# Kernel optimization log

Measured on AMD Instinct MI355X. Metric: run time of the kernel, lower is better.

Reference implementation:

```python
import jax, jax.numpy as jnp
import numpy as np

B, S, D_IN, D_OUT = 4, 2048, 1024, 1024


def setup_inputs() -> dict:
    key = jax.random.key(0)
    k1, k2, k3, k4 = jax.random.split(key, 4)
    scale = 1.0 / np.sqrt(D_IN)
    return {
        "x": jax.random.normal(k1, (B, S, D_IN), dtype=jnp.float32),
        "W_q": jax.random.normal(k2, (D_OUT, D_IN), dtype=jnp.float32) * scale,
        "W_k": jax.random.normal(k3, (D_OUT, D_IN), dtype=jnp.float32) * scale,
        "W_v": jax.random.normal(k4, (D_OUT, D_IN), dtype=jnp.float32) * scale,
    }


def reference(x, W_q, W_k, W_v):
    # torch nn.Linear: y = x @ W.T (bias=False)
    q = jnp.einsum("bsd,od->bso", x, W_q)
    k = jnp.einsum("bsd,od->bso", x, W_k)
    v = jnp.einsum("bsd,od->bso", x, W_v)
    s = q.shape[1]
    scores = jnp.einsum("bqo,bko->bqk", q, k)  # [B, S, S]
    causal = jnp.triu(jnp.ones((s, s), dtype=bool), k=1)
    scores = jnp.where(causal, -jnp.inf, scores)
    inv_sqrt_d = 1.0 / jnp.sqrt(jnp.asarray(q.shape[-1], scores.dtype))
    attn = jax.nn.softmax(scores * inv_sqrt_d, axis=-1)
    # dropout p=0.0 -> identity (deterministic reference)
    return jnp.einsum("bqk,bko->bqo", attn, v)
```

## Files before the change

### kernel.cpp

```cpp
#include <hip/hip_runtime.h>

typedef unsigned short u16;
typedef __bf16 bf16x8 __attribute__((ext_vector_type(8)));
typedef float f32x4 __attribute__((ext_vector_type(4)));

#define AS1 __attribute__((address_space(1)))
#define AS3 __attribute__((address_space(3)))

__device__ inline u16 f2bf(float f) {
  union { float f; unsigned u; } a; a.f = f;
  unsigned u = a.u;
  return (u16)((u + 0x7fffu + ((u >> 16) & 1u)) >> 16);
}

__global__ __launch_bounds__(256) void cvt_kernel(const float* __restrict__ in,
                                                  u16* __restrict__ out) {
  size_t i = ((size_t)blockIdx.x * 256 + threadIdx.x) * 4;
  float4 v = *(const float4*)(in + i);
  ushort4 o;
  o.x = f2bf(v.x); o.y = f2bf(v.y); o.z = f2bf(v.z); o.w = f2bf(v.w);
  *(ushort4*)(out + i) = o;
}

__global__ __launch_bounds__(256) void cvt3_kernel(
    const float* __restrict__ a, const float* __restrict__ b, const float* __restrict__ c,
    u16* __restrict__ oa, u16* __restrict__ ob, u16* __restrict__ oc) {
  int bid = blockIdx.x;
  const float* in; u16* out;
  if (bid < 1024) { in = a; out = oa; }
  else if (bid < 2048) { in = b; out = ob; bid -= 1024; }
  else { in = c; out = oc; bid -= 2048; }
  size_t i = ((size_t)bid * 256 + threadIdx.x) * 4;
  float4 v = *(const float4*)(in + i);
  ushort4 o;
  o.x = f2bf(v.x); o.y = f2bf(v.y); o.z = f2bf(v.z); o.w = f2bf(v.w);
  *(ushort4*)(out + i) = o;
}

template <typename CT>
__device__ __forceinline__ void gemm_core(
    const u16* __restrict__ A, const u16* __restrict__ B, CT* __restrict__ C,
    int nt, int lda, int ldb, int ldc, int m0, int n0, bool atom) {
  __shared__ __align__(16) u16 lds[65536];

  const int tid = threadIdx.x;
  const int ln = tid & 63, wv = tid >> 6;
  const int wr = wv >> 2, wc = wv & 3;

  auto stage = [&](const u16* src, int ld, int t, int h, int ldsbase) {
#pragma unroll
    for (int i = 0; i < 2; ++i) {
      const int c = h * 1024 + i * 512 + tid;
      const int row = c >> 3, slot = c & 7;
      const int col = (slot ^ (row & 7)) * 8;
      __builtin_amdgcn_global_load_lds(
          (const AS1 void*)(src + (size_t)row * ld + (size_t)t * 64 + col),
          (AS3 void*)(&lds[ldsbase + c * 8]), 16, 0, 0);
    }
  };

  f32x4 acc[8][4] = {};

  stage(B, ldb, 0, 0, 32768); stage(B, ldb, 0, 1, 32768);
  stage(A, lda, 0, 0, 0);     stage(A, lda, 0, 1, 0);
  if (nt > 1) {
    stage(B, ldb, 1, 0, 32768 + 16384); stage(B, ldb, 1, 1, 32768 + 16384);
    stage(A, lda, 1, 0, 16384);         stage(A, lda, 1, 1, 16384);
    asm volatile("s_waitcnt vmcnt(8)" ::: "memory");
  } else {
    asm volatile("s_waitcnt vmcnt(0)" ::: "memory");
  }
  __builtin_amdgcn_s_barrier();

  for (int t = 0; t < nt; ++t) {
    const int p = t & 1;
    const u16* La = &lds[p * 16384];
    const u16* Lb = &lds[32768 + p * 16384];
    bf16x8 bfr[4][2];
#pragma unroll
    for (int q = 0; q < 4; ++q) {
      if (q == 0) {
        __builtin_amdgcn_sched_barrier(0);
#pragma unroll
        for (int ni = 0; ni < 4; ++ni)
#pragma unroll
          for (int ks = 0; ks < 2; ++ks) {
            const int row = wc * 64 + ni * 16 + (ln & 15);
            const int kc = ks * 4 + (ln >> 4);
            bfr[ni][ks] = *(const bf16x8*)&Lb[row * 64 + ((kc ^ (row & 7)) << 3)];
          }
      }
      bf16x8 afr[2][2];
#pragma unroll
      for (int mi = 0; mi < 2; ++mi)
#pragma unroll
        for (int ks = 0; ks < 2; ++ks) {
          const int row = wr * 128 + (q * 2 + mi) * 16 + (ln & 15);
          const int kc = ks * 4 + (ln >> 4);
          afr[mi][ks] = *(const bf16x8*)&La[row * 64 + ((kc ^ (row & 7)) << 3)];
        }
      if (q == 0)      { if (t >= 1 && t + 1 < nt) stage(A, lda, t + 1, 0, (p ^ 1) * 16384); }
      else if (q == 1) { if (t >= 1 && t + 1 < nt) stage(A, lda, t + 1, 1, (p ^ 1) * 16384); }
      else if (q == 2) { if (t + 2 < nt) stage(B, ldb, t + 2, 0, 32768 + p * 16384); }
      else             { if (t + 2 < nt) stage(B, ldb, t + 2, 1, 32768 + p * 16384); }

      __builtin_amdgcn_s_barrier();
      __builtin_amdgcn_s_setprio(1);
#pragma unroll
      for (int mi = 0; mi < 2; ++mi)
#pragma unroll
        for (int ni = 0; ni < 4; ++ni)
#pragma unroll
          for (int ks = 0; ks < 2; ++ks)
            acc[q * 2 + mi][ni] = __builtin_amdgcn_mfma_f32_16x16x32_bf16(
                afr[mi][ks], bfr[ni][ks], acc[q * 2 + mi][ni], 0, 0, 0);
      __builtin_amdgcn_s_setprio(0);
      if (q == 3) {
        if (t + 2 < nt)      asm volatile("s_waitcnt vmcnt(4)" ::: "memory");
        else if (t + 1 < nt) asm volatile("s_waitcnt vmcnt(0)" ::: "memory");
      }
      __builtin_amdgcn_s_barrier();
    }
  }

#pragma unroll
  for (int mi = 0; mi < 8; ++mi) {
    const int rbase = m0 + wr * 128 + mi * 16 + (ln >> 4) * 4;
#pragma unroll
    for (int ni = 0; ni < 4; ++ni) {
      const int col = n0 + wc * 64 + ni * 16 + (ln & 15);
#pragma unroll
      for (int r = 0; r < 4; ++r) {
        const float v = acc[mi][ni][r];
        CT* ptr = &C[(size_t)(rbase + r) * ldc + col];
        if constexpr (sizeof(CT) == 4) {
          if (atom) atomicAdd((float*)ptr, v);
          else *(float*)ptr = v;
        } else {
          *ptr = f2bf(v);
        }
      }
    }
  }
}

__global__ __launch_bounds__(512, 2) void proj_kernel(
    const u16* __restrict__ xb, const u16* __restrict__ wqb,
    const u16* __restrict__ wkb, const u16* __restrict__ wvb,
    u16* __restrict__ Qb, u16* __restrict__ Kb, u16* __restrict__ VTb) {
  const int bid = blockIdx.x;
  const u16 *A, *B;
  u16* C;
  int ldc, m0, n0;
  if (bid < 256) {
    const int w = bid >> 7, r = bid & 127;
    m0 = (r >> 2) * 256; n0 = (r & 3) * 256;
    A = xb; B = w ? wkb : wqb; C = w ? Kb : Qb; ldc = 1024;
  } else {
    int r = bid - 256;
    const int z = r >> 5; r &= 31;
    m0 = (r >> 3) * 256; n0 = (r & 7) * 256;
    A = wvb; B = xb + (size_t)z * 2048 * 1024; C = VTb + (size_t)z * 1024 * 2048;
    ldc = 2048;
  }
  gemm_core<u16>(A + (size_t)m0 * 1024, B + (size_t)n0 * 1024, C, 16, 1024, 1024, ldc, m0, n0, false);
}

__global__ __launch_bounds__(512, 2) void qkt_kernel(
    const u16* __restrict__ Qb, const u16* __restrict__ Kb, float* __restrict__ Sb) {
  const int x = blockIdx.x;
  int mi = 0;
  while ((mi + 1) * (mi + 2) / 2 <= x) ++mi;
  const int ni = x - mi * (mi + 1) / 2;
  const int m0 = mi * 256, n0 = ni * 256;
  const u16* A = Qb + (size_t)blockIdx.y * 2048 * 1024 + (size_t)m0 * 1024;
  const u16* B = Kb + (size_t)blockIdx.y * 2048 * 1024 + (size_t)n0 * 1024;
  float* C = Sb + (size_t)blockIdx.y * 2048 * 2048;
  gemm_core<float>(A, B, C, 16, 1024, 1024, 2048, m0, n0, false);
}

__global__ __launch_bounds__(512, 2) void pv_kernel(
    const u16* __restrict__ P, const u16* __restrict__ VTb, float* __restrict__ out) {
  const int c = blockIdx.x;
  int m, k0, ntc; bool atom;
  if (c < 4) { m = c; k0 = 0; ntc = 4 * (c + 1); atom = false; }
  else {
    const int j = c - 4;
    m = 4 + (j >> 1);
    const int nth = 2 * (m + 1);
    k0 = (j & 1) * nth; ntc = nth; atom = true;
  }
  const int m0 = m * 256, n0 = blockIdx.y * 256;
  const u16* A = P + (size_t)blockIdx.z * 2048 * 4096 + (size_t)m0 * 4096 + (size_t)k0 * 64;
  const u16* B = VTb + (size_t)blockIdx.z * 1024 * 2048 + (size_t)n0 * 2048 + (size_t)k0 * 64;
  float* C = out + (size_t)blockIdx.z * 2048 * 1024;
  gemm_core<float>(A, B, C, ntc, 4096, 2048, 1024, m0, n0, atom);
}

__global__ __launch_bounds__(256) void softmax_kernel(float* __restrict__ S, float scale) {
  const int q = blockIdx.x;
  float* row = S + ((size_t)blockIdx.y * 2048 + q) * 2048;
  const int t = threadIdx.x;
  float4 v0 = *(const float4*)(row + t * 4);
  float4 v1 = *(const float4*)(row + 1024 + t * 4);
  float x[8] = {v0.x, v0.y, v0.z, v0.w, v1.x, v1.y, v1.z, v1.w};
  float m = -3.4e38f;
#pragma unroll
  for (int i = 0; i < 8; ++i) {
    const int j = (i < 4) ? (t * 4 + i) : (1024 + t * 4 + (i - 4));
    x[i] = (j <= q) ? x[i] * scale : -3.4e38f;
    m = fmaxf(m, x[i]);
  }
#pragma unroll
  for (int off = 32; off > 0; off >>= 1) m = fmaxf(m, __shfl_xor(m, off, 64));
  __shared__ float redm[4], reds[4];
  const int ln = t & 63, wv = t >> 6;
  if (ln == 0) redm[wv] = m;
  __syncthreads();
  m = fmaxf(fmaxf(redm[0], redm[1]), fmaxf(redm[2], redm[3]));

  float p[8];
  float s = 0.f;
#pragma unroll
  for (int i = 0; i < 8; ++i) {
    p[i] = __expf(x[i] - m);
    s += p[i];
  }
#pragma unroll
  for (int off = 32; off > 0; off >>= 1) s += __shfl_xor(s, off, 64);
  if (ln == 0) reds[wv] = s;
  __syncthreads();
  s = reds[0] + reds[1] + reds[2] + reds[3];
  const float r = 1.0f / s;

  u16* prow = (u16*)row;
  ushort4 o0, o1;
  o0.x = f2bf(p[0] * r); o0.y = f2bf(p[1] * r); o0.z = f2bf(p[2] * r); o0.w = f2bf(p[3] * r);
  o1.x = f2bf(p[4] * r); o1.y = f2bf(p[5] * r); o1.z = f2bf(p[6] * r); o1.w = f2bf(p[7] * r);
  *(ushort4*)(prow + t * 4) = o0;
  *(ushort4*)(prow + 1024 + t * 4) = o1;
}

extern "C" void kernel_launch(void* const* d_in, const int* in_sizes, int n_in,
                              void* d_out, int out_size, void* d_ws, size_t ws_size,
                              hipStream_t stream) {
  const float* x  = (const float*)d_in[0];
  const float* Wq = (const float*)d_in[1];
  const float* Wk = (const float*)d_in[2];
  const float* Wv = (const float*)d_in[3];
  float* out = (float*)d_out;

  char* ws = (char*)d_ws;
  u16* xb   = (u16*)(ws);
  u16* wqb  = (u16*)(ws + (16ul << 20));
  u16* wkb  = (u16*)(ws + (18ul << 20));
  u16* wvb  = (u16*)(ws + (20ul << 20));
  u16* Qb   = (u16*)(ws + (22ul << 20));
  u16* Kb   = (u16*)(ws + (38ul << 20));
  u16* VTb  = (u16*)(ws + (54ul << 20));
  float* Sb = (float*)(ws + (70ul << 20));

  hipMemsetAsync(out, 0, (size_t)out_size * 4, stream);

  cvt_kernel<<<8192, 256, 0, stream>>>(x, xb);
  cvt3_kernel<<<3072, 256, 0, stream>>>(Wq, Wk, Wv, wqb, wkb, wvb);

  proj_kernel<<<384, 512, 0, stream>>>(xb, wqb, wkb, wvb, Qb, Kb, VTb);

  qkt_kernel<<<dim3(36, 4), 512, 0, stream>>>(Qb, Kb, Sb);

  softmax_kernel<<<dim3(2048, 4), 256, 0, stream>>>(Sb, 0.03125f);

  pv_kernel<<<dim3(12, 4, 4), 512, 0, stream>>>((const u16*)Sb, VTb, out);
}
```

Baseline: 175.6 us.

## Split V projection into a 128-row-tile kernel and trim causal softmax and memset work

The GEMM core is templated on the M tile size (256 or 128) so LDS buffers, staging sweeps, wait counts and accumulators scale with it. The V^T projection moves into its own kernel with 128-row tiles, giving 256 blocks instead of 128. The aim is better CU load balance than the previous 384-block combined launch. Softmax rows with q<1024 no longer load or write the upper half, which the causal PV kernel never reads. The output memset now clears only the rows that are accumulated atomically. In exchange there is one extra kernel launch, and the V tiles are smaller, with less reuse per tile.

```diff
diff --git a/kernel.cpp b/kernel.cpp
--- a/kernel.cpp
+++ b/kernel.cpp
@@ -37,36 +37,41 @@
   *(ushort4*)(out + i) = o;
 }
 
-template <typename CT>
+template <typename CT, int BM>
 __device__ __forceinline__ void gemm_core(
     const u16* __restrict__ A, const u16* __restrict__ B, CT* __restrict__ C,
     int nt, int lda, int ldb, int ldc, int m0, int n0, bool atom) {
-  __shared__ __align__(16) u16 lds[65536];
+  constexpr int ABUF = BM * 64;
+  constexpr int ASW = BM / 64;
+  constexpr int PH_MI = BM / 128;
+  __shared__ __align__(16) u16 lds[2 * ABUF + 32768];
 
   const int tid = threadIdx.x;
   const int ln = tid & 63, wv = tid >> 6;
   const int wr = wv >> 2, wc = wv & 3;
 
-  auto stage = [&](const u16* src, int ld, int t, int h, int ldsbase) {
-#pragma unroll
-    for (int i = 0; i < 2; ++i) {
-      const int c = h * 1024 + i * 512 + tid;
-      const int row = c >> 3, slot = c & 7;
-      const int col = (slot ^ (row & 7)) * 8;
-      __builtin_amdgcn_global_load_lds(
-          (const AS1 void*)(src + (size_t)row * ld + (size_t)t * 64 + col),
-          (AS3 void*)(&lds[ldsbase + c * 8]), 16, 0, 0);
-    }
+  auto sweep = [&](const u16* src, int ld, int t, int s, int base) {
+    const int c = s * 512 + tid;
+    const int row = c >> 3, slot = c & 7;
+    const int col = (slot ^ (row & 7)) * 8;
+    __builtin_amdgcn_global_load_lds(
+        (const AS1 void*)(src + (size_t)row * ld + (size_t)t * 64 + col),
+        (AS3 void*)(&lds[base + c * 8]), 16, 0, 0);
   };
 
-  f32x4 acc[8][4] = {};
-
-  stage(B, ldb, 0, 0, 32768); stage(B, ldb, 0, 1, 32768);
-  stage(A, lda, 0, 0, 0);     stage(A, lda, 0, 1, 0);
+  f32x4 acc[2 * BM / 64][4] = {};
+
+#pragma unroll
+  for (int s = 0; s < 4; ++s) sweep(B, ldb, 0, s, 2 * ABUF);
+#pragma unroll
+  for (int s = 0; s < ASW; ++s) sweep(A, lda, 0, s, 0);
   if (nt > 1) {
-    stage(B, ldb, 1, 0, 32768 + 16384); stage(B, ldb, 1, 1, 32768 + 16384);
-    stage(A, lda, 1, 0, 16384);         stage(A, lda, 1, 1, 16384);
-    asm volatile("s_waitcnt vmcnt(8)" ::: "memory");
+#pragma unroll
+    for (int s = 0; s < 4; ++s) sweep(B, ldb, 1, s, 2 * ABUF + 16384);
+#pragma unroll
+    for (int s = 0; s < ASW; ++s) sweep(A, lda, 1, s, ABUF);
+    if constexpr (ASW == 4) asm volatile("s_waitcnt vmcnt(8)" ::: "memory");
+    else                    asm volatile("s_waitcnt vmcnt(6)" ::: "memory");
   } else {
     asm volatile("s_waitcnt vmcnt(0)" ::: "memory");
   }
@@ -74,8 +79,8 @@
 
   for (int t = 0; t < nt; ++t) {
     const int p = t & 1;
-    const u16* La = &lds[p * 16384];
-    const u16* Lb = &lds[32768 + p * 16384];
+    const u16* La = &lds[p * ABUF];
+    const u16* Lb = &lds[2 * ABUF + p * 16384];
     bf16x8 bfr[4][2];
 #pragma unroll
     for (int q = 0; q < 4; ++q) {
@@ -90,30 +95,36 @@
             bfr[ni][ks] = *(const bf16x8*)&Lb[row * 64 + ((kc ^ (row & 7)) << 3)];
           }
       }
-      bf16x8 afr[2][2];
-#pragma unroll
-      for (int mi = 0; mi < 2; ++mi)
+      bf16x8 afr[PH_MI][2];
+#pragma unroll
+      for (int mi = 0; mi < PH_MI; ++mi)
 #pragma unroll
         for (int ks = 0; ks < 2; ++ks) {
-          const int row = wr * 128 + (q * 2 + mi) * 16 + (ln & 15);
+          const int row = wr * (BM / 2) + (q * PH_MI + mi) * 16 + (ln & 15);
           const int kc = ks * 4 + (ln >> 4);
           afr[mi][ks] = *(const bf16x8*)&La[row * 64 + ((kc ^ (row & 7)) << 3)];
         }
-      if (q == 0)      { if (t >= 1 && t + 1 < nt) stage(A, lda, t + 1, 0, (p ^ 1) * 16384); }
-      else if (q == 1) { if (t >= 1 && t + 1 < nt) stage(A, lda, t + 1, 1, (p ^ 1) * 16384); }
-      else if (q == 2) { if (t + 2 < nt) stage(B, ldb, t + 2, 0, 32768 + p * 16384); }
-      else             { if (t + 2 < nt) stage(B, ldb, t + 2, 1, 32768 + p * 16384); }
+      if constexpr (PH_MI == 2) {
+        if (q == 0)      { if (t >= 1 && t + 1 < nt) { sweep(A, lda, t + 1, 0, (p ^ 1) * ABUF); sweep(A, lda, t + 1, 1, (p ^ 1) * ABUF); } }
+        else if (q == 1) { if (t >= 1 && t + 1 < nt) { sweep(A, lda, t + 1, 2, (p ^ 1) * ABUF); sweep(A, lda, t + 1, 3, (p ^ 1) * ABUF); } }
+        else if (q == 2) { if (t + 2 < nt) { sweep(B, ldb, t + 2, 0, 2 * ABUF + p * 16384); sweep(B, ldb, t + 2, 1, 2 * ABUF + p * 16384); } }
+        else             { if (t + 2 < nt) { sweep(B, ldb, t + 2, 2, 2 * ABUF + p * 16384); sweep(B, ldb, t + 2, 3, 2 * ABUF + p * 16384); } }
+      } else {
+        if (q == 0)      { if (t >= 1 && t + 1 < nt) { sweep(A, lda, t + 1, 0, (p ^ 1) * ABUF); sweep(A, lda, t + 1, 1, (p ^ 1) * ABUF); } }
+        else if (q == 2) { if (t + 2 < nt) { sweep(B, ldb, t + 2, 0, 2 * ABUF + p * 16384); sweep(B, ldb, t + 2, 1, 2 * ABUF + p * 16384); } }
+        else if (q == 3) { if (t + 2 < nt) { sweep(B, ldb, t + 2, 2, 2 * ABUF + p * 16384); sweep(B, ldb, t + 2, 3, 2 * ABUF + p * 16384); } }
+      }
 
       __builtin_amdgcn_s_barrier();
       __builtin_amdgcn_s_setprio(1);
 #pragma unroll
-      for (int mi = 0; mi < 2; ++mi)
+      for (int mi = 0; mi < PH_MI; ++mi)
 #pragma unroll
         for (int ni = 0; ni < 4; ++ni)
 #pragma unroll
           for (int ks = 0; ks < 2; ++ks)
-            acc[q * 2 + mi][ni] = __builtin_amdgcn_mfma_f32_16x16x32_bf16(
-                afr[mi][ks], bfr[ni][ks], acc[q * 2 + mi][ni], 0, 0, 0);
+            acc[q * PH_MI + mi][ni] = __builtin_amdgcn_mfma_f32_16x16x32_bf16(
+                afr[mi][ks], bfr[ni][ks], acc[q * PH_MI + mi][ni], 0, 0, 0);
       __builtin_amdgcn_s_setprio(0);
       if (q == 3) {
         if (t + 2 < nt)      asm volatile("s_waitcnt vmcnt(4)" ::: "memory");
@@ -124,8 +135,8 @@
   }
 
 #pragma unroll
-  for (int mi = 0; mi < 8; ++mi) {
-    const int rbase = m0 + wr * 128 + mi * 16 + (ln >> 4) * 4;
+  for (int mi = 0; mi < 2 * BM / 64; ++mi) {
+    const int rbase = m0 + wr * (BM / 2) + mi * 16 + (ln >> 4) * 4;
 #pragma unroll
     for (int ni = 0; ni < 4; ++ni) {
       const int col = n0 + wc * 64 + ni * 16 + (ln & 15);
@@ -144,26 +155,26 @@
   }
 }
 
-__global__ __launch_bounds__(512, 2) void proj_kernel(
+__global__ __launch_bounds__(512, 2) void proj_qk_kernel(
     const u16* __restrict__ xb, const u16* __restrict__ wqb,
-    const u16* __restrict__ wkb, const u16* __restrict__ wvb,
-    u16* __restrict__ Qb, u16* __restrict__ Kb, u16* __restrict__ VTb) {
+    const u16* __restrict__ wkb, u16* __restrict__ Qb, u16* __restrict__ Kb) {
   const int bid = blockIdx.x;
-  const u16 *A, *B;
-  u16* C;
-  int ldc, m0, n0;
-  if (bid < 256) {
-    const int w = bid >> 7, r = bid & 127;
-    m0 = (r >> 2) * 256; n0 = (r & 3) * 256;
-    A = xb; B = w ? wkb : wqb; C = w ? Kb : Qb; ldc = 1024;
-  } else {
-    int r = bid - 256;
-    const int z = r >> 5; r &= 31;
-    m0 = (r >> 3) * 256; n0 = (r & 7) * 256;
-    A = wvb; B = xb + (size_t)z * 2048 * 1024; C = VTb + (size_t)z * 1024 * 2048;
-    ldc = 2048;
-  }
-  gemm_core<u16>(A + (size_t)m0 * 1024, B + (size_t)n0 * 1024, C, 16, 1024, 1024, ldc, m0, n0, false);
+  const int w = bid >> 7, r = bid & 127;
+  const int m0 = (r >> 2) * 256, n0 = (r & 3) * 256;
+  const u16* B = w ? wkb : wqb;
+  u16* C = w ? Kb : Qb;
+  gemm_core<u16, 256>(xb + (size_t)m0 * 1024, B + (size_t)n0 * 1024, C,
+                      16, 1024, 1024, 1024, m0, n0, false);
+}
+
+__global__ __launch_bounds__(512, 2) void vt_kernel(
+    const u16* __restrict__ wvb, const u16* __restrict__ xb, u16* __restrict__ VTb) {
+  const int z = blockIdx.x >> 6, r = blockIdx.x & 63;
+  const int m0 = (r >> 3) * 128, n0 = (r & 7) * 256;
+  gemm_core<u16, 128>(wvb + (size_t)m0 * 1024,
+                      xb + (size_t)z * 2048 * 1024 + (size_t)n0 * 1024,
+                      VTb + (size_t)z * 1024 * 2048,
+                      16, 1024, 1024, 2048, m0, n0, false);
 }
 
 __global__ __launch_bounds__(512, 2) void qkt_kernel(
@@ -176,7 +187,7 @@
   const u16* A = Qb + (size_t)blockIdx.y * 2048 * 1024 + (size_t)m0 * 1024;
   const u16* B = Kb + (size_t)blockIdx.y * 2048 * 1024 + (size_t)n0 * 1024;
   float* C = Sb + (size_t)blockIdx.y * 2048 * 2048;
-  gemm_core<float>(A, B, C, 16, 1024, 1024, 2048, m0, n0, false);
+  gemm_core<float, 256>(A, B, C, 16, 1024, 1024, 2048, m0, n0, false);
 }
 
 __global__ __launch_bounds__(512, 2) void pv_kernel(
@@ -194,15 +205,16 @@
   const u16* A = P + (size_t)blockIdx.z * 2048 * 4096 + (size_t)m0 * 4096 + (size_t)k0 * 64;
   const u16* B = VTb + (size_t)blockIdx.z * 1024 * 2048 + (size_t)n0 * 2048 + (size_t)k0 * 64;
   float* C = out + (size_t)blockIdx.z * 2048 * 1024;
-  gemm_core<float>(A, B, C, ntc, 4096, 2048, 1024, m0, n0, atom);
+  gemm_core<float, 256>(A, B, C, ntc, 4096, 2048, 1024, m0, n0, atom);
 }
 
 __global__ __launch_bounds__(256) void softmax_kernel(float* __restrict__ S, float scale) {
   const int q = blockIdx.x;
+  const bool full = (q >= 1024);
   float* row = S + ((size_t)blockIdx.y * 2048 + q) * 2048;
   const int t = threadIdx.x;
   float4 v0 = *(const float4*)(row + t * 4);
-  float4 v1 = *(const float4*)(row + 1024 + t * 4);
+  float4 v1 = full ? *(const float4*)(row + 1024 + t * 4) : float4{0, 0, 0, 0};
   float x[8] = {v0.x, v0.y, v0.z, v0.w, v1.x, v1.y, v1.z, v1.w};
   float m = -3.4e38f;
 #pragma unroll
@@ -236,9 +248,11 @@
   u16* prow = (u16*)row;
   ushort4 o0, o1;
   o0.x = f2bf(p[0] * r); o0.y = f2bf(p[1] * r); o0.z = f2bf(p[2] * r); o0.w = f2bf(p[3] * r);
-  o1.x = f2bf(p[4] * r); o1.y = f2bf(p[5] * r); o1.z = f2bf(p[6] * r); o1.w = f2bf(p[7] * r);
   *(ushort4*)(prow + t * 4) = o0;
-  *(ushort4*)(prow + 1024 + t * 4) = o1;
+  if (full) {
+    o1.x = f2bf(p[4] * r); o1.y = f2bf(p[5] * r); o1.z = f2bf(p[6] * r); o1.w = f2bf(p[7] * r);
+    *(ushort4*)(prow + 1024 + t * 4) = o1;
+  }
 }
 
 extern "C" void kernel_launch(void* const* d_in, const int* in_sizes, int n_in,
@@ -260,12 +274,14 @@
   u16* VTb  = (u16*)(ws + (54ul << 20));
   float* Sb = (float*)(ws + (70ul << 20));
 
-  hipMemsetAsync(out, 0, (size_t)out_size * 4, stream);
+  for (int b = 0; b < 4; ++b)
+    hipMemsetAsync(out + ((size_t)b * 2048 + 1024) * 1024, 0, 1024 * 1024 * 4, stream);
 
   cvt_kernel<<<8192, 256, 0, stream>>>(x, xb);
   cvt3_kernel<<<3072, 256, 0, stream>>>(Wq, Wk, Wv, wqb, wkb, wvb);
 
-  proj_kernel<<<384, 512, 0, stream>>>(xb, wqb, wkb, wvb, Qb, Kb, VTb);
+  proj_qk_kernel<<<256, 512, 0, stream>>>(xb, wqb, wkb, Qb, Kb);
+  vt_kernel<<<256, 512, 0, stream>>>(wvb, xb, VTb);
 
   qkt_kernel<<<dim3(36, 4), 512, 0, stream>>>(Qb, Kb, Sb);
 
```

Result: no change. 173.4 us (-1.2%).
